# Optimization experiments

Measured on AMD Instinct MI355X. Metric: run time of the kernel, lower is better.

The kernel has to match this reference:

```python
import jax, jax.numpy as jnp
import numpy as np

HEADS = 16
EMBD = 1024
D_K = EMBD // HEADS


def setup_inputs() -> dict:
    key = jax.random.key(0)
    ks = jax.random.split(key, 9)
    s = 1.0 / np.sqrt(EMBD)
    inp = {
        "x": jax.random.normal(ks[0], (4, 2048, EMBD), dtype=jnp.float32),
        "w_q": jax.random.normal(ks[1], (EMBD, EMBD), dtype=jnp.float32) * s,
        "b_q": jax.random.normal(ks[2], (EMBD,), dtype=jnp.float32) * 0.01,
        "w_k": jax.random.normal(ks[3], (EMBD, EMBD), dtype=jnp.float32) * s,
        "b_k": jax.random.normal(ks[4], (EMBD,), dtype=jnp.float32) * 0.01,
        "w_v": jax.random.normal(ks[5], (EMBD, EMBD), dtype=jnp.float32) * s,
        "b_v": jax.random.normal(ks[6], (EMBD,), dtype=jnp.float32) * 0.01,
        "w_o": jax.random.normal(ks[7], (EMBD, EMBD), dtype=jnp.float32) * s,
        "b_o": jax.random.normal(ks[8], (EMBD,), dtype=jnp.float32) * 0.01,
    }
    return inp


def reference(x, w_q, b_q, w_k, b_k, w_v, b_v, w_o, b_o):
    b, s, e = x.shape
    # Linear layers (torch Linear: x @ W^T + b; weights stored as [out,in] -> here [in,out] already? We store [in,out])
    q = x @ w_q + b_q
    k = x @ w_k + b_k
    v = x @ w_v + b_v
    # reshape to [b, h, s, d_k]
    qh = q.reshape(b, s, HEADS, D_K).transpose(0, 2, 1, 3)
    kh = k.reshape(b, s, HEADS, D_K).transpose(0, 2, 1, 3)
    vh = v.reshape(b, s, HEADS, D_K).transpose(0, 2, 1, 3)
    scores = jnp.einsum('bhqd,bhkd->bhqk', qh, kh) / jnp.sqrt(jnp.asarray(D_K, x.dtype))
    attn = jax.nn.softmax(scores, axis=-1)
    out = jnp.einsum('bhqk,bhkd->bhqd', attn, vh)
    merged = out.transpose(0, 2, 1, 3).reshape(b, s, e)
    return merged @ w_o + b_o
```

## Files before the change

### kernel.cpp

```cpp
#include <hip/hip_runtime.h>
#include <math.h>

#define B 4
#define S 2048
#define E 1024
#define H 16
#define DK 64
#define NROW (B * S)
#define NT (S / 64)

typedef _Float16 half_t;
typedef __attribute__((ext_vector_type(8))) _Float16 half8;
typedef __attribute__((ext_vector_type(4))) _Float16 half4;
typedef __attribute__((ext_vector_type(4))) float f32x4;

__device__ __forceinline__ void gload_lds16(const void* g, void* l) {
    __builtin_amdgcn_global_load_lds((__attribute__((address_space(1))) void*)(g),
                                     (__attribute__((address_space(3))) void*)(l), 16, 0, 0);
}

__device__ __forceinline__ float fast_exp2(float x) {
    return __builtin_amdgcn_exp2f(x);
}

__global__ __launch_bounds__(256)
void cast_x_kernel(const float* __restrict__ x, half_t* __restrict__ xh) {
    const size_t i = ((size_t)blockIdx.x * 256 + threadIdx.x) * 8;
    float4 a = *(const float4*)(x + i);
    float4 b = *(const float4*)(x + i + 4);
    half8 hv;
    hv[0] = (half_t)a.x; hv[1] = (half_t)a.y; hv[2] = (half_t)a.z; hv[3] = (half_t)a.w;
    hv[4] = (half_t)b.x; hv[5] = (half_t)b.y; hv[6] = (half_t)b.z; hv[7] = (half_t)b.w;
    *(half8*)(xh + i) = hv;
}

__global__ __launch_bounds__(256)
void cast_wT_kernel(const float* __restrict__ w0, const float* __restrict__ w1,
                    const float* __restrict__ w2, const float* __restrict__ w3,
                    half_t* __restrict__ o0, half_t* __restrict__ o1,
                    half_t* __restrict__ o2, half_t* __restrict__ o3) {
    __shared__ half_t Ts[64][72];
    const int z = blockIdx.z;
    const float* W = (z == 0) ? w0 : (z == 1) ? w1 : (z == 2) ? w2 : w3;
    half_t*      O = (z == 0) ? o0 : (z == 1) ? o1 : (z == 2) ? o2 : o3;
    const int t  = threadIdx.x;
    const int k0 = blockIdx.y * 64;
    const int n0 = blockIdx.x * 64;
    const int r  = t >> 2;
    const int c0 = (t & 3) * 16;
    const float* p = W + (size_t)(k0 + r) * E + n0 + c0;
    #pragma unroll
    for (int j = 0; j < 16; j += 4) {
        float4 v = *(const float4*)(p + j);
        Ts[c0 + j + 0][r] = (half_t)v.x;
        Ts[c0 + j + 1][r] = (half_t)v.y;
        Ts[c0 + j + 2][r] = (half_t)v.z;
        Ts[c0 + j + 3][r] = (half_t)v.w;
    }
    __syncthreads();
    half_t* q = O + (size_t)(n0 + r) * E + k0 + c0;
    *(uint4*)(q)     = *(const uint4*)&Ts[r][c0];
    *(uint4*)(q + 8) = *(const uint4*)&Ts[r][c0 + 8];
}

__global__ __launch_bounds__(256)
void gemm_qkv_kernel(const half_t* __restrict__ A, const half_t* __restrict__ Bt,
                     const float* __restrict__ b_q, const float* __restrict__ b_k,
                     const float* __restrict__ b_v,
                     half_t* __restrict__ Qh, half_t* __restrict__ Kh,
                     half_t* __restrict__ Vt) {
    __shared__ half_t SMEM[128 * 136];
    half_t* As = SMEM;
    half_t* Bs = SMEM + 8192;
    const int t    = threadIdx.x;
    const int w    = t >> 6;
    const int lane = t & 63;
    const int ln   = t & 15;
    const int qd   = (t >> 4) & 3;
    const int orig = blockIdx.y * 24 + blockIdx.x;
    const int swz  = (orig & 7) * 192 + (orig >> 3);
    const int bn0  = (swz % 24) * 128;
    const int bm0  = (swz / 24) * 128;
    const int wm   = (w & 1) * 64;
    const int wn   = (w >> 1) * 64;
    const int srow = lane >> 2;
    const int sch  = (lane & 3) * 8;

    f32x4 acc[4][4];
    #pragma unroll
    for (int mi = 0; mi < 4; ++mi)
        #pragma unroll
        for (int ni = 0; ni < 4; ++ni) acc[mi][ni] = (f32x4){0.f, 0.f, 0.f, 0.f};

    for (int k0 = 0; k0 < E; k0 += 64) {
        #pragma unroll
        for (int kh = 0; kh < 2; ++kh)
            #pragma unroll
            for (int c = 0; c < 2; ++c) {
                const int rr = c * 64 + w * 16;
                gload_lds16(A  + (size_t)(bm0 + rr + srow) * E + k0 + kh * 32 + sch, As + kh * 4096 + rr * 32);
                gload_lds16(Bt + (size_t)(bn0 + rr + srow) * E + k0 + kh * 32 + sch, Bs + kh * 4096 + rr * 32);
            }
        __syncthreads();
        #pragma unroll
        for (int kh = 0; kh < 2; ++kh) {
            half8 af[4], bf[4];
            #pragma unroll
            for (int mi = 0; mi < 4; ++mi) af[mi] = *(const half8*)&As[kh * 4096 + (wm + mi * 16 + ln) * 32 + qd * 8];
            #pragma unroll
            for (int ni = 0; ni < 4; ++ni) bf[ni] = *(const half8*)&Bs[kh * 4096 + (wn + ni * 16 + ln) * 32 + qd * 8];
            #pragma unroll
            for (int mi = 0; mi < 4; ++mi)
                #pragma unroll
                for (int ni = 0; ni < 4; ++ni)
                    acc[mi][ni] = __builtin_amdgcn_mfma_f32_16x16x32_f16(af[mi], bf[ni], acc[mi][ni], 0, 0, 0);
        }
        __syncthreads();
    }

    const int route = bn0 >> 10;
    const int nloc0 = bn0 & 1023;
    const float* bp = (route == 0) ? b_q : (route == 1) ? b_k : b_v;
    float bv[4];
    #pragma unroll
    for (int ni = 0; ni < 4; ++ni) bv[ni] = bp[nloc0 + wn + ni * 16 + ln];

    if (route < 2) {
        half_t* Cst = (route == 0) ? Qh : Kh;
        #pragma unroll
        for (int mi = 0; mi < 4; ++mi)
            #pragma unroll
            for (int r = 0; r < 4; ++r) {
                const size_t row = (size_t)(bm0 + wm + mi * 16 + qd * 4 + r);
                #pragma unroll
                for (int ni = 0; ni < 4; ++ni)
                    Cst[row * E + nloc0 + wn + ni * 16 + ln] = (half_t)(acc[mi][ni][r] + bv[ni]);
            }
    } else {
        #pragma unroll
        for (int mi = 0; mi < 4; ++mi)
            #pragma unroll
            for (int ni = 0; ni < 4; ++ni)
                #pragma unroll
                for (int r = 0; r < 4; ++r)
                    SMEM[(wn + ni * 16 + ln) * 136 + wm + mi * 16 + qd * 4 + r] =
                        (half_t)(acc[mi][ni][r] + bv[ni]);
        __syncthreads();
        const int nl = t >> 1;
        const int sc = (t & 1) * 64;
        const int gv = nloc0 + nl;
        const int hh = gv >> 6, dd = gv & 63;
        const int bb = bm0 >> 11;
        const int sb = (bm0 & (S - 1)) + sc;
        half_t* dst = Vt + ((size_t)(bb * H + hh) * DK + dd) * S + sb;
        const half_t* src = SMEM + nl * 136 + sc;
        #pragma unroll
        for (int j = 0; j < 64; j += 8)
            *(half8*)(dst + j) = *(const half8*)(src + j);
    }
}

__global__ __launch_bounds__(256)
void gemm_oproj_kernel(const half_t* __restrict__ A, const half_t* __restrict__ Bt,
                       const float* __restrict__ bias, float* __restrict__ Cout) {
    __shared__ half_t As[2][128 * 32];
    __shared__ half_t Bs[2][128 * 32];
    const int t    = threadIdx.x;
    const int w    = t >> 6;
    const int lane = t & 63;
    const int ln   = t & 15;
    const int qd   = (t >> 4) & 3;
    const int orig = blockIdx.y * 8 + blockIdx.x;
    const int swz  = (orig & 7) * 64 + (orig >> 3);
    const int bn0  = (swz & 7) * 128;
    const int bm0  = (swz >> 3) * 128;
    const int wm   = (w & 1) * 64;
    const int wn   = (w >> 1) * 64;
    const int srow = lane >> 2;
    const int sch  = (lane & 3) * 8;

    f32x4 acc[4][4];
    #pragma unroll
    for (int mi = 0; mi < 4; ++mi)
        #pragma unroll
        for (int ni = 0; ni < 4; ++ni) acc[mi][ni] = (f32x4){0.f, 0.f, 0.f, 0.f};

    for (int k0 = 0; k0 < E; k0 += 64) {
        #pragma unroll
        for (int kh = 0; kh < 2; ++kh)
            #pragma unroll
            for (int c = 0; c < 2; ++c) {
                const int rr = c * 64 + w * 16;
                gload_lds16(A  + (size_t)(bm0 + rr + srow) * E + k0 + kh * 32 + sch, &As[kh][rr * 32]);
                gload_lds16(Bt + (size_t)(bn0 + rr + srow) * E + k0 + kh * 32 + sch, &Bs[kh][rr * 32]);
            }
        __syncthreads();
        #pragma unroll
        for (int kh = 0; kh < 2; ++kh) {
            half8 af[4], bf[4];
            #pragma unroll
            for (int mi = 0; mi < 4; ++mi) af[mi] = *(const half8*)&As[kh][(wm + mi * 16 + ln) * 32 + qd * 8];
            #pragma unroll
            for (int ni = 0; ni < 4; ++ni) bf[ni] = *(const half8*)&Bs[kh][(wn + ni * 16 + ln) * 32 + qd * 8];
            #pragma unroll
            for (int mi = 0; mi < 4; ++mi)
                #pragma unroll
                for (int ni = 0; ni < 4; ++ni)
                    acc[mi][ni] = __builtin_amdgcn_mfma_f32_16x16x32_f16(af[mi], bf[ni], acc[mi][ni], 0, 0, 0);
        }
        __syncthreads();
    }

    float bv[4];
    #pragma unroll
    for (int ni = 0; ni < 4; ++ni) bv[ni] = bias[bn0 + wn + ni * 16 + ln];
    #pragma unroll
    for (int mi = 0; mi < 4; ++mi)
        #pragma unroll
        for (int r = 0; r < 4; ++r) {
            const size_t row = (size_t)(bm0 + wm + mi * 16 + qd * 4 + r);
            #pragma unroll
            for (int ni = 0; ni < 4; ++ni)
                Cout[row * E + bn0 + wn + ni * 16 + ln] = acc[mi][ni][r] + bv[ni];
        }
}

__global__ __launch_bounds__(256, 4)
void attn_kernel7(const half_t* __restrict__ Qg, const half_t* __restrict__ Kg,
                  const half_t* __restrict__ Vtg, half_t* __restrict__ CTX) {
    __shared__ half_t Kbuf[2][4096];
    __shared__ half_t Vbuf[2][4096];

    const int t    = threadIdx.x;
    const int w    = t >> 6;
    const int lane = t & 63;
    const int ln   = t & 15;
    const int qd   = (t >> 4) & 3;
    const int orig = blockIdx.y * 16 + blockIdx.x;
    const int swz  = (orig & 7) * 128 + (orig >> 3);
    const int bh   = swz >> 4;
    const int s0   = (swz & 15) * 128;
    const int b    = bh >> 4;
    const int h    = bh & 15;
    const int q0   = w * 32;

    half8 aq[2][2];
    #pragma unroll
    for (int mt = 0; mt < 2; ++mt)
        #pragma unroll
        for (int kd = 0; kd < 2; ++kd)
            aq[mt][kd] = *(const half8*)(Qg +
                (size_t)(b * S + s0 + q0 + mt * 16 + ln) * E + h * DK + kd * 32 + qd * 8);

    const half_t* kgp = Kg + (size_t)(b * S + w * 16 + ln) * E + h * DK + qd * 8;
    const half_t* vgp = Vtg + (size_t)(bh * DK + w * 16 + (lane & 7)) * S + (lane >> 3) * 8;

    gload_lds16(kgp,      &Kbuf[0][(w * 2 + 0) * 512]);
    gload_lds16(kgp + 32, &Kbuf[0][(w * 2 + 1) * 512]);
    gload_lds16(vgp,                 &Vbuf[0][(w * 2 + 0) * 512]);
    gload_lds16(vgp + (size_t)8 * S, &Vbuf[0][(w * 2 + 1) * 512]);

    f32x4 oacc[2][4];
    #pragma unroll
    for (int mt = 0; mt < 2; ++mt)
        #pragma unroll
        for (int dt = 0; dt < 4; ++dt) oacc[mt][dt] = (f32x4){0.f, 0.f, 0.f, 0.f};
    f32x4 lfrag[2];
    lfrag[0] = (f32x4){0.f, 0.f, 0.f, 0.f};
    lfrag[1] = (f32x4){0.f, 0.f, 0.f, 0.f};

    half8 vone;
    #pragma unroll
    for (int j = 0; j < 8; ++j) vone[j] = (half_t)1;

    const float kexp  = 0.1803368731f;
    const float kbias = 7.2134752f;

    const int vrb = (ln >> 3) * 512 + (ln & 7) * 8 + (qd & 1) * 4 + (qd >> 1) * 64;

    for (int kt = 0; kt < NT; ++kt) {
        const int cur = kt & 1;
        __syncthreads();

        if (kt + 1 < NT) {
            const half_t* kp = kgp + (size_t)(kt + 1) * 64 * E;
            const half_t* vp = vgp + (kt + 1) * 64;
            gload_lds16(kp,      &Kbuf[1 - cur][(w * 2 + 0) * 512]);
            gload_lds16(kp + 32, &Kbuf[1 - cur][(w * 2 + 1) * 512]);
            gload_lds16(vp,                 &Vbuf[1 - cur][(w * 2 + 0) * 512]);
            gload_lds16(vp + (size_t)8 * S, &Vbuf[1 - cur][(w * 2 + 1) * 512]);
        }

        half8 kf[4][2];
        #pragma unroll
        for (int ct = 0; ct < 4; ++ct)
            #pragma unroll
            for (int kd = 0; kd < 2; ++kd)
                kf[ct][kd] = *(const half8*)&Kbuf[cur][(ct * 2 + kd) * 512 + lane * 8];

        half8 vf[4][2];
        const half_t* vb = &Vbuf[cur][vrb];
        #pragma unroll
        for (int dt = 0; dt < 4; ++dt)
            #pragma unroll
            for (int kq = 0; kq < 2; ++kq) {
                union { half4 h4[2]; half8 h8; } u;
                u.h4[0] = *(const half4*)(vb + dt * 1024 + kq * 256);
                u.h4[1] = *(const half4*)(vb + dt * 1024 + kq * 256 + 128);
                vf[dt][kq] = u.h8;
            }

        #pragma unroll
        for (int mt = 0; mt < 2; ++mt) {
            f32x4 sacc[4];
            #pragma unroll
            for (int ct = 0; ct < 4; ++ct) {
                f32x4 sv = (f32x4){0.f, 0.f, 0.f, 0.f};
                sv = __builtin_amdgcn_mfma_f32_16x16x32_f16(kf[ct][0], aq[mt][0], sv, 0, 0, 0);
                sv = __builtin_amdgcn_mfma_f32_16x16x32_f16(kf[ct][1], aq[mt][1], sv, 0, 0, 0);
                sacc[ct] = sv;
            }
            half8 pa[2];
            #pragma unroll
            for (int kq = 0; kq < 2; ++kq)
                #pragma unroll
                for (int j = 0; j < 8; ++j) {
                    const int ct = kq * 2 + (j >> 2);
                    const int r  = j & 3;
                    pa[kq][j] = (half_t)fast_exp2(fmaf(sacc[ct][r], kexp, -kbias));
                }

            lfrag[mt] = __builtin_amdgcn_mfma_f32_16x16x32_f16(pa[0], vone, lfrag[mt], 0, 0, 0);
            lfrag[mt] = __builtin_amdgcn_mfma_f32_16x16x32_f16(pa[1], vone, lfrag[mt], 0, 0, 0);
            #pragma unroll
            for (int dt = 0; dt < 4; ++dt) {
                oacc[mt][dt] = __builtin_amdgcn_mfma_f32_16x16x32_f16(pa[0], vf[dt][0], oacc[mt][dt], 0, 0, 0);
                oacc[mt][dt] = __builtin_amdgcn_mfma_f32_16x16x32_f16(pa[1], vf[dt][1], oacc[mt][dt], 0, 0, 0);
            }
        }
    }

    #pragma unroll
    for (int mt = 0; mt < 2; ++mt)
        #pragma unroll
        for (int r = 0; r < 4; ++r) {
            const float invl = 1.f / lfrag[mt][r];
            const size_t row = (size_t)(b * S + s0 + q0 + mt * 16 + qd * 4 + r);
            #pragma unroll
            for (int dt = 0; dt < 4; ++dt)
                CTX[row * E + h * DK + dt * 16 + ln] = (half_t)(oacc[mt][dt][r] * invl);
        }
}

extern "C" void kernel_launch(void* const* d_in, const int* in_sizes, int n_in,
                              void* d_out, int out_size, void* d_ws, size_t ws_size,
                              hipStream_t stream) {
    const float* x   = (const float*)d_in[0];
    const float* w_q = (const float*)d_in[1];
    const float* b_q = (const float*)d_in[2];
    const float* w_k = (const float*)d_in[3];
    const float* b_k = (const float*)d_in[4];
    const float* w_v = (const float*)d_in[5];
    const float* b_v = (const float*)d_in[6];
    const float* w_o = (const float*)d_in[7];
    const float* b_o = (const float*)d_in[8];
    float* out = (float*)d_out;

    half_t* xh  = (half_t*)d_ws;
    half_t* Wt3 = xh  + (size_t)NROW * E;
    half_t* WtO = Wt3 + (size_t)3 * E * E;
    half_t* Qh  = WtO + (size_t)E * E;
    half_t* Kh  = Qh  + (size_t)NROW * E;
    half_t* Vt  = Kh  + (size_t)NROW * E;
    half_t* CTX = Vt  + (size_t)NROW * E;

    cast_x_kernel<<<dim3(NROW * E / (256 * 8)), dim3(256), 0, stream>>>(x, xh);
    cast_wT_kernel<<<dim3(16, 16, 4), dim3(256), 0, stream>>>(
        w_q, w_k, w_v, w_o,
        Wt3, Wt3 + (size_t)E * E, Wt3 + (size_t)2 * E * E, WtO);

    gemm_qkv_kernel<<<dim3(3 * E / 128, NROW / 128), dim3(256), 0, stream>>>(
        xh, Wt3, b_q, b_k, b_v, Qh, Kh, Vt);

    attn_kernel7<<<dim3(S / 128, B * H), dim3(256), 0, stream>>>(Qh, Kh, Vt, CTX);

    gemm_oproj_kernel<<<dim3(E / 128, NROW / 128), dim3(256), 0, stream>>>(CTX, WtO, b_o, out);
}
```

Baseline: 281.9 us.

## Triple-buffer GEMM LDS tiles with async prefetch and fragment-ordered layout

Both projection GEMMs now run a three-stage ring of 32-wide K tiles in LDS. Loads for tile kt+2 are issued while tile kt is being computed, and a partial vmcnt wait plus a single barrier per step replaces the two full syncthreads per iteration. The LDS layout is also rearranged so each lane's MFMA fragment sits at lane*8 in contiguous 512-element blocks, which makes fragment reads conflict-free and linear. The cost is more LDS per block (48KB), which could lower occupancy, plus reliance on hand-written waitcnt counts being correct.

```diff
diff --git a/kernel.cpp b/kernel.cpp
--- a/kernel.cpp
+++ b/kernel.cpp
@@ -8,6 +8,7 @@
 #define DK 64
 #define NROW (B * S)
 #define NT (S / 64)
+#define NKT (E / 32)
 
 typedef _Float16 half_t;
 typedef __attribute__((ext_vector_type(8))) _Float16 half8;
@@ -69,9 +70,7 @@
                      const float* __restrict__ b_v,
                      half_t* __restrict__ Qh, half_t* __restrict__ Kh,
                      half_t* __restrict__ Vt) {
-    __shared__ half_t SMEM[128 * 136];
-    half_t* As = SMEM;
-    half_t* Bs = SMEM + 8192;
+    __shared__ half_t SM[3 * 8192];
     const int t    = threadIdx.x;
     const int w    = t >> 6;
     const int lane = t & 63;
@@ -83,8 +82,11 @@
     const int bm0  = (swz / 24) * 128;
     const int wm   = (w & 1) * 64;
     const int wn   = (w >> 1) * 64;
-    const int srow = lane >> 2;
-    const int sch  = (lane & 3) * 8;
+
+    const half_t* Ag = A  + (size_t)(bm0 + w * 32 + ln) * E + ((lane >> 4) * 8);
+    const half_t* Bg = Bt + (size_t)(bn0 + w * 32 + ln) * E + ((lane >> 4) * 8);
+    half_t* Al = SM + (w * 2) * 512;
+    half_t* Bl = SM + 4096 + (w * 2) * 512;
 
     f32x4 acc[4][4];
     #pragma unroll
@@ -92,31 +94,40 @@
         #pragma unroll
         for (int ni = 0; ni < 4; ++ni) acc[mi][ni] = (f32x4){0.f, 0.f, 0.f, 0.f};
 
-    for (int k0 = 0; k0 < E; k0 += 64) {
-        #pragma unroll
-        for (int kh = 0; kh < 2; ++kh)
-            #pragma unroll
-            for (int c = 0; c < 2; ++c) {
-                const int rr = c * 64 + w * 16;
-                gload_lds16(A  + (size_t)(bm0 + rr + srow) * E + k0 + kh * 32 + sch, As + kh * 4096 + rr * 32);
-                gload_lds16(Bt + (size_t)(bn0 + rr + srow) * E + k0 + kh * 32 + sch, Bs + kh * 4096 + rr * 32);
-            }
-        __syncthreads();
-        #pragma unroll
-        for (int kh = 0; kh < 2; ++kh) {
-            half8 af[4], bf[4];
-            #pragma unroll
-            for (int mi = 0; mi < 4; ++mi) af[mi] = *(const half8*)&As[kh * 4096 + (wm + mi * 16 + ln) * 32 + qd * 8];
-            #pragma unroll
-            for (int ni = 0; ni < 4; ++ni) bf[ni] = *(const half8*)&Bs[kh * 4096 + (wn + ni * 16 + ln) * 32 + qd * 8];
-            #pragma unroll
-            for (int mi = 0; mi < 4; ++mi)
-                #pragma unroll
-                for (int ni = 0; ni < 4; ++ni)
-                    acc[mi][ni] = __builtin_amdgcn_mfma_f32_16x16x32_f16(af[mi], bf[ni], acc[mi][ni], 0, 0, 0);
-        }
-        __syncthreads();
-    }
+    #pragma unroll
+    for (int p = 0; p < 2; ++p) {
+        gload_lds16(Ag + p * 32,                Al + p * 8192);
+        gload_lds16(Ag + (size_t)16 * E + p * 32, Al + p * 8192 + 512);
+        gload_lds16(Bg + p * 32,                Bl + p * 8192);
+        gload_lds16(Bg + (size_t)16 * E + p * 32, Bl + p * 8192 + 512);
+    }
+
+    for (int kt = 0; kt < NKT; ++kt) {
+        if (kt < NKT - 1) asm volatile("s_waitcnt vmcnt(4)" ::: "memory");
+        else              asm volatile("s_waitcnt vmcnt(0)" ::: "memory");
+        __builtin_amdgcn_s_barrier();
+        if (kt + 2 < NKT) {
+            const int sb = (kt + 2) % 3;
+            gload_lds16(Ag + kt * 32 + 64,                Al + sb * 8192);
+            gload_lds16(Ag + (size_t)16 * E + kt * 32 + 64, Al + sb * 8192 + 512);
+            gload_lds16(Bg + kt * 32 + 64,                Bl + sb * 8192);
+            gload_lds16(Bg + (size_t)16 * E + kt * 32 + 64, Bl + sb * 8192 + 512);
+        }
+        const int cur = kt % 3;
+        const half_t* Ar = SM + cur * 8192 + (wm >> 4) * 512 + lane * 8;
+        const half_t* Br = SM + cur * 8192 + 4096 + (wn >> 4) * 512 + lane * 8;
+        half8 af[4], bf[4];
+        #pragma unroll
+        for (int mi = 0; mi < 4; ++mi) af[mi] = *(const half8*)(Ar + mi * 512);
+        #pragma unroll
+        for (int ni = 0; ni < 4; ++ni) bf[ni] = *(const half8*)(Br + ni * 512);
+        #pragma unroll
+        for (int mi = 0; mi < 4; ++mi)
+            #pragma unroll
+            for (int ni = 0; ni < 4; ++ni)
+                acc[mi][ni] = __builtin_amdgcn_mfma_f32_16x16x32_f16(af[mi], bf[ni], acc[mi][ni], 0, 0, 0);
+    }
+    __syncthreads();
 
     const int route = bn0 >> 10;
     const int nloc0 = bn0 & 1023;
@@ -143,7 +154,7 @@
             for (int ni = 0; ni < 4; ++ni)
                 #pragma unroll
                 for (int r = 0; r < 4; ++r)
-                    SMEM[(wn + ni * 16 + ln) * 136 + wm + mi * 16 + qd * 4 + r] =
+                    SM[(wn + ni * 16 + ln) * 136 + wm + mi * 16 + qd * 4 + r] =
                         (half_t)(acc[mi][ni][r] + bv[ni]);
         __syncthreads();
         const int nl = t >> 1;
@@ -153,7 +164,7 @@
         const int bb = bm0 >> 11;
         const int sb = (bm0 & (S - 1)) + sc;
         half_t* dst = Vt + ((size_t)(bb * H + hh) * DK + dd) * S + sb;
-        const half_t* src = SMEM + nl * 136 + sc;
+        const half_t* src = SM + nl * 136 + sc;
         #pragma unroll
         for (int j = 0; j < 64; j += 8)
             *(half8*)(dst + j) = *(const half8*)(src + j);
@@ -163,8 +174,7 @@
 __global__ __launch_bounds__(256)
 void gemm_oproj_kernel(const half_t* __restrict__ A, const half_t* __restrict__ Bt,
                        const float* __restrict__ bias, float* __restrict__ Cout) {
-    __shared__ half_t As[2][128 * 32];
-    __shared__ half_t Bs[2][128 * 32];
+    __shared__ half_t SM[3 * 8192];
     const int t    = threadIdx.x;
     const int w    = t >> 6;
     const int lane = t & 63;
@@ -176,8 +186,11 @@
     const int bm0  = (swz >> 3) * 128;
     const int wm   = (w & 1) * 64;
     const int wn   = (w >> 1) * 64;
-    const int srow = lane >> 2;
-    const int sch  = (lane & 3) * 8;
+
+    const half_t* Ag = A  + (size_t)(bm0 + w * 32 + ln) * E + ((lane >> 4) * 8);
+    const half_t* Bg = Bt + (size_t)(bn0 + w * 32 + ln) * E + ((lane >> 4) * 8);
+    half_t* Al = SM + (w * 2) * 512;
+    half_t* Bl = SM + 4096 + (w * 2) * 512;
 
     f32x4 acc[4][4];
     #pragma unroll
@@ -185,30 +198,38 @@
         #pragma unroll
         for (int ni = 0; ni < 4; ++ni) acc[mi][ni] = (f32x4){0.f, 0.f, 0.f, 0.f};
 
-    for (int k0 = 0; k0 < E; k0 += 64) {
-        #pragma unroll
-        for (int kh = 0; kh < 2; ++kh)
-            #pragma unroll
-            for (int c = 0; c < 2; ++c) {
-                const int rr = c * 64 + w * 16;
-                gload_lds16(A  + (size_t)(bm0 + rr + srow) * E + k0 + kh * 32 + sch, &As[kh][rr * 32]);
-                gload_lds16(Bt + (size_t)(bn0 + rr + srow) * E + k0 + kh * 32 + sch, &Bs[kh][rr * 32]);
-            }
-        __syncthreads();
-        #pragma unroll
-        for (int kh = 0; kh < 2; ++kh) {
-            half8 af[4], bf[4];
-            #pragma unroll
-            for (int mi = 0; mi < 4; ++mi) af[mi] = *(const half8*)&As[kh][(wm + mi * 16 + ln) * 32 + qd * 8];
-            #pragma unroll
-            for (int ni = 0; ni < 4; ++ni) bf[ni] = *(const half8*)&Bs[kh][(wn + ni * 16 + ln) * 32 + qd * 8];
-            #pragma unroll
-            for (int mi = 0; mi < 4; ++mi)
-                #pragma unroll
-                for (int ni = 0; ni < 4; ++ni)
-                    acc[mi][ni] = __builtin_amdgcn_mfma_f32_16x16x32_f16(af[mi], bf[ni], acc[mi][ni], 0, 0, 0);
-        }
-        __syncthreads();
+    #pragma unroll
+    for (int p = 0; p < 2; ++p) {
+        gload_lds16(Ag + p * 32,                Al + p * 8192);
+        gload_lds16(Ag + (size_t)16 * E + p * 32, Al + p * 8192 + 512);
+        gload_lds16(Bg + p * 32,                Bl + p * 8192);
+        gload_lds16(Bg + (size_t)16 * E + p * 32, Bl + p * 8192 + 512);
+    }
+
+    for (int kt = 0; kt < NKT; ++kt) {
+        if (kt < NKT - 1) asm volatile("s_waitcnt vmcnt(4)" ::: "memory");
+        else              asm volatile("s_waitcnt vmcnt(0)" ::: "memory");
+        __builtin_amdgcn_s_barrier();
+        if (kt + 2 < NKT) {
+            const int sb = (kt + 2) % 3;
+            gload_lds16(Ag + kt * 32 + 64,                Al + sb * 8192);
+            gload_lds16(Ag + (size_t)16 * E + kt * 32 + 64, Al + sb * 8192 + 512);
+            gload_lds16(Bg + kt * 32 + 64,                Bl + sb * 8192);
+            gload_lds16(Bg + (size_t)16 * E + kt * 32 + 64, Bl + sb * 8192 + 512);
+        }
+        const int cur = kt % 3;
+        const half_t* Ar = SM + cur * 8192 + (wm >> 4) * 512 + lane * 8;
+        const half_t* Br = SM + cur * 8192 + 4096 + (wn >> 4) * 512 + lane * 8;
+        half8 af[4], bf[4];
+        #pragma unroll
+        for (int mi = 0; mi < 4; ++mi) af[mi] = *(const half8*)(Ar + mi * 512);
+        #pragma unroll
+        for (int ni = 0; ni < 4; ++ni) bf[ni] = *(const half8*)(Br + ni * 512);
+        #pragma unroll
+        for (int mi = 0; mi < 4; ++mi)
+            #pragma unroll
+            for (int ni = 0; ni < 4; ++ni)
+                acc[mi][ni] = __builtin_amdgcn_mfma_f32_16x16x32_f16(af[mi], bf[ni], acc[mi][ni], 0, 0, 0);
     }
 
     float bv[4];
```

Measured after the change: 313.9 us. 11.3% more time.
